# Kernel optimization log

Measured on AMD Instinct MI355X. Metric: run time of the kernel, lower is better.

## Reference

```python
import jax, jax.numpy as jnp
import numpy as np

B = 512       # batch_size
IN = 256      # input_size
H = 512       # hidden_size
OUT = 64      # output_size
N_PAIRS = B - 1   # number of H0 persistence deaths (connected components merges)
TOL = 1e-6    # rtol for torch.isclose
ATOL = 1e-8   # torch default atol
EPS = 0.0     # homology_eps
TARGET_P = 1.0
HOM_P = 1.0
COMP_P = 0.01

_IU = np.triu_indices(B, 1)  # condensed pdist indexing, static


def _mlp(batch, W1, b1, W2, b2, W3, b3, Wout, bout):
    # FeedForward: input->hidden, (n_layers-1) hidden->hidden, hidden->output, ReLU
    h = jax.nn.relu(batch @ W1 + b1)
    h = jax.nn.relu(h @ W2 + b2)
    h = jax.nn.relu(h @ W3 + b3)
    return h @ Wout + bout


def _pdist(y):
    # condensed euclidean pairwise distances, same ordering as torch F.pdist
    d = y[_IU[0]] - y[_IU[1]]                 # [P, OUT]
    return jnp.sqrt(jnp.sum(d * d, axis=-1))  # [P]


def setup_inputs() -> dict:
    key = jax.random.key(0)
    ks = jax.random.split(key, 8)
    batch = jax.random.normal(ks[0], (B, IN), jnp.float32)
    target = jax.random.normal(ks[1], (B, OUT), jnp.float32)
    W1 = jax.random.normal(ks[2], (IN, H), jnp.float32) / np.sqrt(IN)
    W2 = jax.random.normal(ks[3], (H, H), jnp.float32) / np.sqrt(H)
    W3 = jax.random.normal(ks[4], (H, H), jnp.float32) / np.sqrt(H)
    Wout = jax.random.normal(ks[5], (H, OUT), jnp.float32) / np.sqrt(H)
    b1 = jnp.zeros((H,), jnp.float32)
    b2 = jnp.zeros((H,), jnp.float32)
    b3 = jnp.zeros((H,), jnp.float32)
    bout = jnp.zeros((OUT,), jnp.float32)
    # persistence deaths = actual critical pdist values (from the external
    # Vietoris-Rips routine in the original); sample N_PAIRS distinct entries.
    y0 = _mlp(batch, W1, b1, W2, b2, W3, b3, Wout, bout)
    pd0 = np.asarray(_pdist(y0))
    idx = np.random.default_rng(0).choice(pd0.shape[0], N_PAIRS, replace=False)
    persistence_deaths = jnp.asarray(pd0[idx], jnp.float32)
    return {"batch": batch, "target": target,
            "W1": W1, "b1": b1, "W2": W2, "b2": b2, "W3": W3, "b3": b3,
            "Wout": Wout, "bout": bout,
            "persistence_deaths": persistence_deaths}


def reference(batch, target, W1, b1, W2, b2, W3, b3, Wout, bout, persistence_deaths):
    y = _mlp(batch, W1, b1, W2, b2, W3, b3, Wout, bout)   # [B, OUT]
    y_hom = y  # normalize_for_homology = False
    pd = _pdist(y_hom)                                     # [P]
    # vectorized indicator_death over all pairs (replaces per-pair Python loop)
    mask = jnp.any(jnp.isclose(pd[:, None], persistence_deaths[None, :],
                               rtol=TOL, atol=ATOL), axis=1)      # [P] bool
    # homology_dim=0: birth_pdist = 0; norm=1 of selected (death - 0 + eps)
    homology_loss = jnp.sum(jnp.abs(jnp.where(mask, pd + EPS, 0.0)))
    target_loss = jnp.mean((target - y) ** 2)
    compactness_loss = jnp.sum(jnp.abs(y - jnp.mean(y, axis=0, keepdims=True)))
    loss = TARGET_P * target_loss + HOM_P * homology_loss + COMP_P * compactness_loss
    return loss
```

## Files before the change

### kernel.cpp

```cpp
#include <hip/hip_runtime.h>

#define B_    512
#define IN_   256
#define H_    512
#define OUT_  64
#define NDEATH (B_ - 1)
#define NSORT  512
#define RTOL_ 1e-6
#define ATOL_ 1e-8
#define NBLK  256
#define KT    32

typedef __attribute__((ext_vector_type(4))) double d4_t;

__device__ __forceinline__ void ast(double* p, double v) {
    __hip_atomic_store(p, v, __ATOMIC_RELAXED, __HIP_MEMORY_SCOPE_AGENT);
}

__device__ __forceinline__ void gbar(unsigned* cnt, unsigned nb, bool wait) {
    __syncthreads();
    if (threadIdx.x == 0) {
        __hip_atomic_fetch_add(cnt, 1u, __ATOMIC_RELAXED,
                               __HIP_MEMORY_SCOPE_AGENT);
        if (wait) {
            while (__hip_atomic_load(cnt, __ATOMIC_RELAXED,
                                     __HIP_MEMORY_SCOPE_AGENT) < nb)
                __builtin_amdgcn_s_sleep(2);
        }
    }
    __syncthreads();
}

__device__ void sort_windows(const float* __restrict__ deaths,
                             double* sd, double* slo, double* shi, int t) {
    int i1 = t + 256;
    sd[t]  = (t  < NDEATH) ? (double)deaths[t]  : 1e300;
    sd[i1] = (i1 < NDEATH) ? (double)deaths[i1] : 1e300;
    __syncthreads();
    for (int k = 2; k <= NSORT; k <<= 1) {
        for (int j = k >> 1; j > 0; j >>= 1) {
            int l = ((t & ~(j - 1)) << 1) | (t & (j - 1));
            int p = l + j;
            bool up = ((l & k) == 0);
            double a = sd[l], b = sd[p];
            if ((a > b) == up) { sd[l] = b; sd[p] = a; }
            __syncthreads();
        }
    }
    for (int i = t; i < NSORT; i += 256) {
        double d = sd[i];
        double w = ATOL_ + RTOL_ * fabs(d);
        slo[i] = d - w;
        shi[i] = d + w;
    }
    __syncthreads();
}

template <typename TIN, bool RELU>
__device__ void gemm_dev(const TIN* __restrict__ A, const float* __restrict__ W,
                         const float* __restrict__ bias, double* __restrict__ C,
                         int N, int K, int bid, int t,
                         double (&As)[2][KT][33], double (&Ws)[2][KT][33]) {
    const int lane = t & 63;
    const int wave = t >> 6;
    const int wm   = wave & 1, wn = wave >> 1;
    const int nbx  = N >> 5;
    const int row0 = (bid / nbx) << 5;
    const int col0 = (bid % nbx) << 5;

    const int akk = t & 31;
    const int amm = t >> 5;
    const int wnn = t & 31;
    const int wkk = t >> 5;
    const int nkt = K >> 5;

    TIN   ar[2][4];
    float wr[2][4];

    auto load_to = [&](int rs, int kt) {
        const int k0 = kt << 5;
        #pragma unroll
        for (int p = 0; p < 4; ++p) {
            ar[rs][p] = A[(size_t)(row0 + amm + 8 * p) * K + k0 + akk];
            wr[rs][p] = W[(size_t)(k0 + wkk + 8 * p) * N + col0 + wnn];
        }
    };
    auto stage = [&](int rs, int buf) {
        #pragma unroll
        for (int p = 0; p < 4; ++p) {
            As[buf][akk][amm + 8 * p] = (double)ar[rs][p];
            Ws[buf][wkk + 8 * p][wnn] = (double)wr[rs][p];
        }
    };

    load_to(0, 0);
    if (nkt > 1) load_to(1, 1);
    stage(0, 0);
    __syncthreads();

    d4_t c4 = {0.0, 0.0, 0.0, 0.0};
    const int mrow = wm * 16 + (lane & 15);
    const int ncol = wn * 16 + (lane & 15);
    const int kq   = lane >> 4;

    for (int kt = 0; kt < nkt; ++kt) {
        const int cur = kt & 1;
        if (kt + 2 < nkt) load_to(cur, kt + 2);
        #pragma unroll
        for (int ks = 0; ks < KT / 4; ++ks) {
            double av = As[cur][ks * 4 + kq][mrow];
            double bv = Ws[cur][ks * 4 + kq][ncol];
            c4 = __builtin_amdgcn_mfma_f64_16x16x4f64(av, bv, c4, 0, 0, 0);
        }
        __syncthreads();
        if (kt + 1 < nkt) stage(cur ^ 1, cur ^ 1);
        __syncthreads();
    }

    #pragma unroll
    for (int r = 0; r < 4; ++r) {
        int row = row0 + wm * 16 + (lane >> 4) * 4 + r;
        int col = col0 + wn * 16 + (lane & 15);
        double v = c4[r] + (double)bias[col];
        if (RELU) v = v > 0.0 ? v : 0.0;
        ast(&C[(size_t)row * N + col], v);
    }
}

__device__ void mc_dev(const float* __restrict__ target,
                       const double* __restrict__ y,
                       double* __restrict__ t_part, double* __restrict__ c_part,
                       int c, int t) {
    const int wave = t >> 6, lane = t & 63;
    double v0 = y[(size_t)t * OUT_ + c];
    double v1 = y[(size_t)(t + 256) * OUT_ + c];
    double s = v0 + v1;
    for (int off = 32; off; off >>= 1) s += __shfl_down(s, off);
    __shared__ double swm[4];
    __shared__ double smean;
    if (lane == 0) swm[wave] = s;
    __syncthreads();
    if (t == 0) smean = (swm[0] + swm[1] + swm[2] + swm[3]) / (double)B_;
    __syncthreads();
    double m = smean;
    double d0 = (double)target[(size_t)t * OUT_ + c] - v0;
    double d1 = (double)target[(size_t)(t + 256) * OUT_ + c] - v1;
    double t_s = d0 * d0 + d1 * d1;
    double c_s = fabs(v0 - m) + fabs(v1 - m);
    for (int off = 32; off; off >>= 1) {
        t_s += __shfl_down(t_s, off);
        c_s += __shfl_down(c_s, off);
    }
    __shared__ double st[4], sc[4];
    if (lane == 0) { st[wave] = t_s; sc[wave] = c_s; }
    __syncthreads();
    if (t == 0) {
        ast(&t_part[c], st[0] + st[1] + st[2] + st[3]);
        ast(&c_part[c], sc[0] + sc[1] + sc[2] + sc[3]);
    }
}

__device__ __forceinline__ double pair_val(const double* __restrict__ yrow_s,
                                           const double* __restrict__ yj,
                                           const double* __restrict__ slo,
                                           const double* __restrict__ shi) {
    double s = 0.0;
    #pragma unroll
    for (int d = 0; d < OUT_; d += 2) {
        double2 v = *(const double2*)(yj + d);
        double d0 = yrow_s[d]     - v.x;
        double d1 = yrow_s[d + 1] - v.y;
        s = fma(d0, d0, s);
        s = fma(d1, d1, s);
    }
    double pd = sqrt(s);
    int pos = 0;
    #pragma unroll
    for (int step = NSORT / 2; step; step >>= 1) {
        if (slo[pos + step - 1] <= pd) pos += step;
    }
    bool m = (pos > 0) && (shi[pos - 1] >= pd);
    return m ? pd : 0.0;
}

__device__ void pdist_dev(const double* __restrict__ y,
                          double* __restrict__ hom_part, int bid, int t,
                          double* yA, double* yB,
                          const double* slo, const double* shi) {
    const int iA = bid;
    const int iB = 510 - bid;
    if (t < OUT_)            yA[t]        = y[(size_t)iA * OUT_ + t];
    else if (t < 2 * OUT_)   yB[t - OUT_] = y[(size_t)iB * OUT_ + (t - OUT_)];
    __syncthreads();

    double local = 0.0;
    for (int j = iA + 1 + t; j < B_; j += 256)
        local += pair_val(yA, y + (size_t)j * OUT_, slo, shi);
    if (iB != iA)
        for (int j = iB + 1 + t; j < B_; j += 256)
            local += pair_val(yB, y + (size_t)j * OUT_, slo, shi);

    for (int off = 32; off; off >>= 1) local += __shfl_down(local, off);
    __shared__ double sw[4];
    int wave = t >> 6, lane = t & 63;
    if (lane == 0) sw[wave] = local;
    __syncthreads();
    if (t == 0) ast(&hom_part[bid], sw[0] + sw[1] + sw[2] + sw[3]);
}

__global__ __launch_bounds__(256) void fused_k(
    const float* __restrict__ batch, const float* __restrict__ target,
    const float* __restrict__ W1, const float* __restrict__ b1,
    const float* __restrict__ W2, const float* __restrict__ b2,
    const float* __restrict__ W3, const float* __restrict__ b3,
    const float* __restrict__ Wout, const float* __restrict__ bout,
    const float* __restrict__ deaths, float* __restrict__ out,
    double* __restrict__ hA, double* __restrict__ hB,
    double* __restrict__ hC, double* __restrict__ yv,
    double* __restrict__ hom_part, double* __restrict__ t_part,
    double* __restrict__ c_part, unsigned* __restrict__ cnt) {
    const int bid = blockIdx.x;
    const int t   = threadIdx.x;

    __shared__ double As[2][KT][33];
    __shared__ double Ws[2][KT][33];
    __shared__ double slo[NSORT], shi[NSORT];
    __shared__ double yA[OUT_], yB[OUT_];
    double* sd = &As[0][0][0];

    gemm_dev<float,  true>(batch, W1, b1, hA, H_, IN_, bid, t, As, Ws);
    gbar(&cnt[0], NBLK, true);
    gemm_dev<double, true>(hA, W2, b2, hB, H_, H_, bid, t, As, Ws);
    gbar(&cnt[1], NBLK, true);
    gemm_dev<double, true>(hB, W3, b3, hC, H_, H_, bid, t, As, Ws);
    gbar(&cnt[2], NBLK, true);

    if (bid < 32) gemm_dev<double, false>(hC, Wout, bout, yv, OUT_, H_, bid, t, As, Ws);
    else          sort_windows(deaths, sd, slo, shi, t);
    gbar(&cnt[3], NBLK, true);
    if (bid < 32) sort_windows(deaths, sd, slo, shi, t);

    pdist_dev(yv, hom_part, bid, t, yA, yB, slo, shi);
    if (bid < OUT_) mc_dev(target, yv, t_part, c_part, bid, t);

    gbar(&cnt[4], NBLK, bid == 0);
    if (bid == 0) {
        double h  = __hip_atomic_load(&hom_part[t], __ATOMIC_RELAXED,
                                      __HIP_MEMORY_SCOPE_AGENT);
        double tp = 0.0, cp = 0.0;
        if (t < OUT_) {
            tp = __hip_atomic_load(&t_part[t], __ATOMIC_RELAXED,
                                   __HIP_MEMORY_SCOPE_AGENT);
            cp = __hip_atomic_load(&c_part[t], __ATOMIC_RELAXED,
                                   __HIP_MEMORY_SCOPE_AGENT);
        }
        for (int off = 32; off; off >>= 1) {
            h  += __shfl_down(h,  off);
            tp += __shfl_down(tp, off);
            cp += __shfl_down(cp, off);
        }
        __shared__ double sh[4], stp[4], scp[4];
        int wave = t >> 6, lane = t & 63;
        if (lane == 0) { sh[wave] = h; stp[wave] = tp; scp[wave] = cp; }
        __syncthreads();
        if (t == 0) {
            double hs = sh[0]  + sh[1]  + sh[2]  + sh[3];
            double ts = stp[0] + stp[1] + stp[2] + stp[3];
            double cs = scp[0] + scp[1] + scp[2] + scp[3];
            out[0] = (float)(ts / (double)(B_ * OUT_) + hs + 0.01 * cs);
        }
    }
}

extern "C" void kernel_launch(void* const* d_in, const int* in_sizes, int n_in,
                              void* d_out, int out_size, void* d_ws, size_t ws_size,
                              hipStream_t stream) {
    const float* batch  = (const float*)d_in[0];
    const float* target = (const float*)d_in[1];
    const float* W1     = (const float*)d_in[2];
    const float* b1     = (const float*)d_in[3];
    const float* W2     = (const float*)d_in[4];
    const float* b2     = (const float*)d_in[5];
    const float* W3     = (const float*)d_in[6];
    const float* b3     = (const float*)d_in[7];
    const float* Wout   = (const float*)d_in[8];
    const float* bout   = (const float*)d_in[9];
    const float* deaths = (const float*)d_in[10];
    float* out = (float*)d_out;

    double* hA       = (double*)d_ws;
    double* hB       = hA + (size_t)B_ * H_;
    double* hC       = hB + (size_t)B_ * H_;
    double* yv       = hC + (size_t)B_ * H_;
    double* hom_part = yv + (size_t)B_ * OUT_;
    double* t_part   = hom_part + NBLK;
    double* c_part   = t_part + OUT_;
    unsigned* cnt    = (unsigned*)(c_part + OUT_);

    hipMemsetAsync(cnt, 0, 8 * sizeof(unsigned), stream);

    fused_k<<<dim3(NBLK), dim3(256), 0, stream>>>(
        batch, target, W1, b1, W2, b2, W3, b3, Wout, bout, deaths, out,
        hA, hB, hC, yv, hom_part, t_part, c_part, cnt);
}
```

Baseline: 142.3 us.

## Double block size to 512 threads with split-K MFMA across wave groups

```diff
diff --git a/kernel.cpp b/kernel.cpp
--- a/kernel.cpp
+++ b/kernel.cpp
@@ -9,7 +9,7 @@
 #define RTOL_ 1e-6
 #define ATOL_ 1e-8
 #define NBLK  256
-#define KT    32
+#define KT    64
 
 typedef __attribute__((ext_vector_type(4))) double d4_t;
 
@@ -17,42 +17,37 @@
     __hip_atomic_store(p, v, __ATOMIC_RELAXED, __HIP_MEMORY_SCOPE_AGENT);
 }
 
-__device__ __forceinline__ void gbar(unsigned* cnt, unsigned nb, bool wait) {
+__device__ __forceinline__ void gbar(unsigned* cnt, unsigned nb) {
     __syncthreads();
     if (threadIdx.x == 0) {
         __hip_atomic_fetch_add(cnt, 1u, __ATOMIC_RELAXED,
                                __HIP_MEMORY_SCOPE_AGENT);
-        if (wait) {
-            while (__hip_atomic_load(cnt, __ATOMIC_RELAXED,
-                                     __HIP_MEMORY_SCOPE_AGENT) < nb)
-                __builtin_amdgcn_s_sleep(2);
-        }
+        while (__hip_atomic_load(cnt, __ATOMIC_RELAXED,
+                                 __HIP_MEMORY_SCOPE_AGENT) < nb)
+            __builtin_amdgcn_s_sleep(2);
     }
     __syncthreads();
 }
 
 __device__ void sort_windows(const float* __restrict__ deaths,
                              double* sd, double* slo, double* shi, int t) {
-    int i1 = t + 256;
-    sd[t]  = (t  < NDEATH) ? (double)deaths[t]  : 1e300;
-    sd[i1] = (i1 < NDEATH) ? (double)deaths[i1] : 1e300;
+    sd[t] = (t < NDEATH) ? (double)deaths[t] : 1e300;
     __syncthreads();
     for (int k = 2; k <= NSORT; k <<= 1) {
         for (int j = k >> 1; j > 0; j >>= 1) {
-            int l = ((t & ~(j - 1)) << 1) | (t & (j - 1));
-            int p = l + j;
-            bool up = ((l & k) == 0);
-            double a = sd[l], b = sd[p];
-            if ((a > b) == up) { sd[l] = b; sd[p] = a; }
+            int ixj = t ^ j;
+            if (ixj > t) {
+                double a = sd[t], b = sd[ixj];
+                bool up = ((t & k) == 0);
+                if ((a > b) == up) { sd[t] = b; sd[ixj] = a; }
+            }
             __syncthreads();
         }
     }
-    for (int i = t; i < NSORT; i += 256) {
-        double d = sd[i];
-        double w = ATOL_ + RTOL_ * fabs(d);
-        slo[i] = d - w;
-        shi[i] = d + w;
-    }
+    double d = sd[t];
+    double w = ATOL_ + RTOL_ * fabs(d);
+    slo[t] = d - w;
+    shi[t] = d + w;
     __syncthreads();
 }
 
@@ -63,33 +58,35 @@
                          double (&As)[2][KT][33], double (&Ws)[2][KT][33]) {
     const int lane = t & 63;
     const int wave = t >> 6;
-    const int wm   = wave & 1, wn = wave >> 1;
+    const int wg   = wave >> 2;
+    const int wv   = wave & 3;
+    const int wm   = wv & 1, wn = wv >> 1;
     const int nbx  = N >> 5;
     const int row0 = (bid / nbx) << 5;
     const int col0 = (bid % nbx) << 5;
 
-    const int akk = t & 31;
-    const int amm = t >> 5;
+    const int akk = t & 63;
+    const int amm = t >> 6;
     const int wnn = t & 31;
     const int wkk = t >> 5;
-    const int nkt = K >> 5;
+    const int nkt = K >> 6;
 
     TIN   ar[2][4];
     float wr[2][4];
 
     auto load_to = [&](int rs, int kt) {
-        const int k0 = kt << 5;
+        const int k0 = kt << 6;
         #pragma unroll
         for (int p = 0; p < 4; ++p) {
             ar[rs][p] = A[(size_t)(row0 + amm + 8 * p) * K + k0 + akk];
-            wr[rs][p] = W[(size_t)(k0 + wkk + 8 * p) * N + col0 + wnn];
+            wr[rs][p] = W[(size_t)(k0 + wkk + 16 * p) * N + col0 + wnn];
         }
     };
     auto stage = [&](int rs, int buf) {
         #pragma unroll
         for (int p = 0; p < 4; ++p) {
-            As[buf][akk][amm + 8 * p] = (double)ar[rs][p];
-            Ws[buf][wkk + 8 * p][wnn] = (double)wr[rs][p];
+            As[buf][akk][amm + 8 * p]  = (double)ar[rs][p];
+            Ws[buf][wkk + 16 * p][wnn] = (double)wr[rs][p];
         }
     };
 
@@ -99,17 +96,18 @@
     __syncthreads();
 
     d4_t c4 = {0.0, 0.0, 0.0, 0.0};
-    const int mrow = wm * 16 + (lane & 15);
-    const int ncol = wn * 16 + (lane & 15);
-    const int kq   = lane >> 4;
+    const int mrow  = wm * 16 + (lane & 15);
+    const int ncol  = wn * 16 + (lane & 15);
+    const int kq    = lane >> 4;
+    const int kbase = wg * 32;
 
     for (int kt = 0; kt < nkt; ++kt) {
         const int cur = kt & 1;
         if (kt + 2 < nkt) load_to(cur, kt + 2);
         #pragma unroll
-        for (int ks = 0; ks < KT / 4; ++ks) {
-            double av = As[cur][ks * 4 + kq][mrow];
-            double bv = Ws[cur][ks * 4 + kq][ncol];
+        for (int ks = 0; ks < 8; ++ks) {
+            double av = As[cur][kbase + ks * 4 + kq][mrow];
+            double bv = Ws[cur][kbase + ks * 4 + kq][ncol];
             c4 = __builtin_amdgcn_mfma_f64_16x16x4f64(av, bv, c4, 0, 0, 0);
         }
         __syncthreads();
@@ -117,46 +115,58 @@
         __syncthreads();
     }
 
-    #pragma unroll
-    for (int r = 0; r < 4; ++r) {
-        int row = row0 + wm * 16 + (lane >> 4) * 4 + r;
-        int col = col0 + wn * 16 + (lane & 15);
-        double v = c4[r] + (double)bias[col];
-        if (RELU) v = v > 0.0 ? v : 0.0;
-        ast(&C[(size_t)row * N + col], v);
-    }
+    double* cs = &As[0][0][0];
+    if (wg == 1) {
+        #pragma unroll
+        for (int r = 0; r < 4; ++r) cs[((wv * 64 + lane) << 2) + r] = c4[r];
+    }
+    __syncthreads();
+    if (wg == 0) {
+        #pragma unroll
+        for (int r = 0; r < 4; ++r) {
+            int row = row0 + wm * 16 + (lane >> 4) * 4 + r;
+            int col = col0 + wn * 16 + (lane & 15);
+            double v = c4[r] + cs[((wv * 64 + lane) << 2) + r];
+            v += (double)bias[col];
+            if (RELU) v = v > 0.0 ? v : 0.0;
+            ast(&C[(size_t)row * N + col], v);
+        }
+    }
+    __syncthreads();
 }
 
 __device__ void mc_dev(const float* __restrict__ target,
                        const double* __restrict__ y,
                        double* __restrict__ t_part, double* __restrict__ c_part,
-                       int c, int t) {
+                       int c, int t, double* red) {
     const int wave = t >> 6, lane = t & 63;
-    double v0 = y[(size_t)t * OUT_ + c];
-    double v1 = y[(size_t)(t + 256) * OUT_ + c];
-    double s = v0 + v1;
+    double v = y[(size_t)t * OUT_ + c];
+    double s = v;
     for (int off = 32; off; off >>= 1) s += __shfl_down(s, off);
-    __shared__ double swm[4];
     __shared__ double smean;
-    if (lane == 0) swm[wave] = s;
-    __syncthreads();
-    if (t == 0) smean = (swm[0] + swm[1] + swm[2] + swm[3]) / (double)B_;
+    if (lane == 0) red[wave] = s;
+    __syncthreads();
+    if (t == 0) {
+        double m = 0.0;
+        for (int w = 0; w < 8; ++w) m += red[w];
+        smean = m / (double)B_;
+    }
     __syncthreads();
     double m = smean;
-    double d0 = (double)target[(size_t)t * OUT_ + c] - v0;
-    double d1 = (double)target[(size_t)(t + 256) * OUT_ + c] - v1;
-    double t_s = d0 * d0 + d1 * d1;
-    double c_s = fabs(v0 - m) + fabs(v1 - m);
+    double d = (double)target[(size_t)t * OUT_ + c] - v;
+    double t_s = d * d;
+    double c_s = fabs(v - m);
     for (int off = 32; off; off >>= 1) {
         t_s += __shfl_down(t_s, off);
         c_s += __shfl_down(c_s, off);
     }
-    __shared__ double st[4], sc[4];
-    if (lane == 0) { st[wave] = t_s; sc[wave] = c_s; }
+    if (lane == 0) { red[wave] = t_s; red[8 + wave] = c_s; }
     __syncthreads();
     if (t == 0) {
-        ast(&t_part[c], st[0] + st[1] + st[2] + st[3]);
-        ast(&c_part[c], sc[0] + sc[1] + sc[2] + sc[3]);
+        double ts = 0.0, cs = 0.0;
+        for (int w = 0; w < 8; ++w) { ts += red[w]; cs += red[8 + w]; }
+        ast(&t_part[c], ts);
+        ast(&c_part[c], cs);
     }
 }
 
@@ -186,7 +196,7 @@
 __device__ void pdist_dev(const double* __restrict__ y,
                           double* __restrict__ hom_part, int bid, int t,
                           double* yA, double* yB,
-                          const double* slo, const double* shi) {
+                          const double* slo, const double* shi, double* red) {
     const int iA = bid;
     const int iB = 510 - bid;
     if (t < OUT_)            yA[t]        = y[(size_t)iA * OUT_ + t];
@@ -194,21 +204,24 @@
     __syncthreads();
 
     double local = 0.0;
-    for (int j = iA + 1 + t; j < B_; j += 256)
+    for (int j = iA + 1 + t; j < B_; j += 512)
         local += pair_val(yA, y + (size_t)j * OUT_, slo, shi);
     if (iB != iA)
-        for (int j = iB + 1 + t; j < B_; j += 256)
+        for (int j = iB + 1 + t; j < B_; j += 512)
             local += pair_val(yB, y + (size_t)j * OUT_, slo, shi);
 
     for (int off = 32; off; off >>= 1) local += __shfl_down(local, off);
-    __shared__ double sw[4];
     int wave = t >> 6, lane = t & 63;
-    if (lane == 0) sw[wave] = local;
-    __syncthreads();
-    if (t == 0) ast(&hom_part[bid], sw[0] + sw[1] + sw[2] + sw[3]);
-}
-
-__global__ __launch_bounds__(256) void fused_k(
+    if (lane == 0) red[wave] = local;
+    __syncthreads();
+    if (t == 0) {
+        double s = 0.0;
+        for (int w = 0; w < 8; ++w) s += red[w];
+        ast(&hom_part[bid], s);
+    }
+}
+
+__global__ __launch_bounds__(512) void fused_k(
     const float* __restrict__ batch, const float* __restrict__ target,
     const float* __restrict__ W1, const float* __restrict__ b1,
     const float* __restrict__ W2, const float* __restrict__ b2,
@@ -226,27 +239,35 @@
     __shared__ double Ws[2][KT][33];
     __shared__ double slo[NSORT], shi[NSORT];
     __shared__ double yA[OUT_], yB[OUT_];
+    __shared__ double red[16];
+    __shared__ int    lastf;
     double* sd = &As[0][0][0];
 
     gemm_dev<float,  true>(batch, W1, b1, hA, H_, IN_, bid, t, As, Ws);
-    gbar(&cnt[0], NBLK, true);
+    gbar(&cnt[0], NBLK);
     gemm_dev<double, true>(hA, W2, b2, hB, H_, H_, bid, t, As, Ws);
-    gbar(&cnt[1], NBLK, true);
+    gbar(&cnt[1], NBLK);
     gemm_dev<double, true>(hB, W3, b3, hC, H_, H_, bid, t, As, Ws);
-    gbar(&cnt[2], NBLK, true);
+    gbar(&cnt[2], NBLK);
 
     if (bid < 32) gemm_dev<double, false>(hC, Wout, bout, yv, OUT_, H_, bid, t, As, Ws);
     else          sort_windows(deaths, sd, slo, shi, t);
-    gbar(&cnt[3], NBLK, true);
+    gbar(&cnt[3], NBLK);
     if (bid < 32) sort_windows(deaths, sd, slo, shi, t);
 
-    pdist_dev(yv, hom_part, bid, t, yA, yB, slo, shi);
-    if (bid < OUT_) mc_dev(target, yv, t_part, c_part, bid, t);
-
-    gbar(&cnt[4], NBLK, bid == 0);
-    if (bid == 0) {
-        double h  = __hip_atomic_load(&hom_part[t], __ATOMIC_RELAXED,
-                                      __HIP_MEMORY_SCOPE_AGENT);
+    pdist_dev(yv, hom_part, bid, t, yA, yB, slo, shi, red);
+    if (bid < OUT_) mc_dev(target, yv, t_part, c_part, bid, t, red);
+
+    __syncthreads();
+    if (t == 0) {
+        unsigned prev = __hip_atomic_fetch_add(&cnt[4], 1u, __ATOMIC_RELAXED,
+                                               __HIP_MEMORY_SCOPE_AGENT);
+        lastf = (prev == NBLK - 1);
+    }
+    __syncthreads();
+    if (lastf) {
+        double h  = (t < NBLK) ? __hip_atomic_load(&hom_part[t], __ATOMIC_RELAXED,
+                                                   __HIP_MEMORY_SCOPE_AGENT) : 0.0;
         double tp = 0.0, cp = 0.0;
         if (t < OUT_) {
             tp = __hip_atomic_load(&t_part[t], __ATOMIC_RELAXED,
@@ -259,14 +280,16 @@
             tp += __shfl_down(tp, off);
             cp += __shfl_down(cp, off);
         }
-        __shared__ double sh[4], stp[4], scp[4];
         int wave = t >> 6, lane = t & 63;
-        if (lane == 0) { sh[wave] = h; stp[wave] = tp; scp[wave] = cp; }
+        if (lane == 0) { red[wave] = h; red[8 + wave] = tp + cp * 0.0; }
+        __shared__ double red2[16];
+        if (lane == 0) { red2[wave] = tp; red2[8 + wave] = cp; }
         __syncthreads();
         if (t == 0) {
-            double hs = sh[0]  + sh[1]  + sh[2]  + sh[3];
-            double ts = stp[0] + stp[1] + stp[2] + stp[3];
-            double cs = scp[0] + scp[1] + scp[2] + scp[3];
+            double hs = 0.0, ts = 0.0, cs = 0.0;
+            for (int w = 0; w < 8; ++w) {
+                hs += red[w]; ts += red2[w]; cs += red2[8 + w];
+            }
             out[0] = (float)(ts / (double)(B_ * OUT_) + hs + 0.01 * cs);
         }
     }
@@ -299,7 +322,7 @@
 
     hipMemsetAsync(cnt, 0, 8 * sizeof(unsigned), stream);
 
-    fused_k<<<dim3(NBLK), dim3(256), 0, stream>>>(
+    fused_k<<<dim3(NBLK), dim3(512), 0, stream>>>(
         batch, target, W1, b1, W2, b2, W3, b3, Wout, bout, deaths, out,
         hA, hB, hC, yv, hom_part, t_part, c_part, cnt);
 }
```

Result: slower. 145.9 us (+2.5%).

## Replace grid-wide barriers between MLP layers with per-row-band group barriers

Applied to the files above, without the earlier changes.

```diff
diff --git a/kernel.cpp b/kernel.cpp
--- a/kernel.cpp
+++ b/kernel.cpp
@@ -17,16 +17,14 @@
     __hip_atomic_store(p, v, __ATOMIC_RELAXED, __HIP_MEMORY_SCOPE_AGENT);
 }
 
-__device__ __forceinline__ void gbar(unsigned* cnt, unsigned nb, bool wait) {
+__device__ __forceinline__ void gbar(unsigned* cnt, unsigned nb) {
     __syncthreads();
     if (threadIdx.x == 0) {
         __hip_atomic_fetch_add(cnt, 1u, __ATOMIC_RELAXED,
                                __HIP_MEMORY_SCOPE_AGENT);
-        if (wait) {
-            while (__hip_atomic_load(cnt, __ATOMIC_RELAXED,
-                                     __HIP_MEMORY_SCOPE_AGENT) < nb)
-                __builtin_amdgcn_s_sleep(2);
-        }
+        while (__hip_atomic_load(cnt, __ATOMIC_RELAXED,
+                                 __HIP_MEMORY_SCOPE_AGENT) < nb)
+            __builtin_amdgcn_s_sleep(2);
     }
     __syncthreads();
 }
@@ -59,14 +57,14 @@
 template <typename TIN, bool RELU>
 __device__ void gemm_dev(const TIN* __restrict__ A, const float* __restrict__ W,
                          const float* __restrict__ bias, double* __restrict__ C,
-                         int N, int K, int bid, int t,
+                         int N, int K, int tile, int t,
                          double (&As)[2][KT][33], double (&Ws)[2][KT][33]) {
     const int lane = t & 63;
     const int wave = t >> 6;
     const int wm   = wave & 1, wn = wave >> 1;
     const int nbx  = N >> 5;
-    const int row0 = (bid / nbx) << 5;
-    const int col0 = (bid % nbx) << 5;
+    const int row0 = (tile / nbx) << 5;
+    const int col0 = (tile % nbx) << 5;
 
     const int akk = t & 31;
     const int amm = t >> 5;
@@ -221,30 +219,41 @@
     double* __restrict__ c_part, unsigned* __restrict__ cnt) {
     const int bid = blockIdx.x;
     const int t   = threadIdx.x;
+    const int g   = bid >> 4;
+    const int c   = bid & 15;
+    unsigned* gc  = cnt + g * 32;
 
     __shared__ double As[2][KT][33];
     __shared__ double Ws[2][KT][33];
     __shared__ double slo[NSORT], shi[NSORT];
     __shared__ double yA[OUT_], yB[OUT_];
+    __shared__ int    lastf;
     double* sd = &As[0][0][0];
 
     gemm_dev<float,  true>(batch, W1, b1, hA, H_, IN_, bid, t, As, Ws);
-    gbar(&cnt[0], NBLK, true);
+    gbar(&gc[0], 16);
     gemm_dev<double, true>(hA, W2, b2, hB, H_, H_, bid, t, As, Ws);
-    gbar(&cnt[1], NBLK, true);
+    gbar(&gc[1], 16);
     gemm_dev<double, true>(hB, W3, b3, hC, H_, H_, bid, t, As, Ws);
-    gbar(&cnt[2], NBLK, true);
-
-    if (bid < 32) gemm_dev<double, false>(hC, Wout, bout, yv, OUT_, H_, bid, t, As, Ws);
-    else          sort_windows(deaths, sd, slo, shi, t);
-    gbar(&cnt[3], NBLK, true);
-    if (bid < 32) sort_windows(deaths, sd, slo, shi, t);
+    gbar(&gc[2], 16);
+
+    if (c < 2) gemm_dev<double, false>(hC, Wout, bout, yv, OUT_, H_, g * 2 + c, t, As, Ws);
+    else       sort_windows(deaths, sd, slo, shi, t);
+
+    gbar(&cnt[512], NBLK);
+    if (c < 2) sort_windows(deaths, sd, slo, shi, t);
 
     pdist_dev(yv, hom_part, bid, t, yA, yB, slo, shi);
     if (bid < OUT_) mc_dev(target, yv, t_part, c_part, bid, t);
 
-    gbar(&cnt[4], NBLK, bid == 0);
-    if (bid == 0) {
+    __syncthreads();
+    if (t == 0) {
+        unsigned prev = __hip_atomic_fetch_add(&cnt[544], 1u, __ATOMIC_RELAXED,
+                                               __HIP_MEMORY_SCOPE_AGENT);
+        lastf = (prev == NBLK - 1);
+    }
+    __syncthreads();
+    if (lastf) {
         double h  = __hip_atomic_load(&hom_part[t], __ATOMIC_RELAXED,
                                       __HIP_MEMORY_SCOPE_AGENT);
         double tp = 0.0, cp = 0.0;
@@ -297,7 +306,7 @@
     double* c_part   = t_part + OUT_;
     unsigned* cnt    = (unsigned*)(c_part + OUT_);
 
-    hipMemsetAsync(cnt, 0, 8 * sizeof(unsigned), stream);
+    hipMemsetAsync(cnt, 0, 576 * sizeof(unsigned), stream);
 
     fused_k<<<dim3(NBLK), dim3(256), 0, stream>>>(
         batch, target, W1, b1, W2, b2, W3, b3, Wout, bout, deaths, out,
```

Result: faster. 131.7 us (median of 2 runs) (-7.4%).
